# Optimization experiments

Measured on AMD Instinct MI355X. Metric: run time of the kernel, lower is better.

Reference implementation:

```python
import jax, jax.numpy as jnp
import numpy as np


def quantize_ternary(w):
    # BitNet b1.58 absmean ternary quantization: clip(round(w/gamma), -1, 1) * gamma
    gamma = jnp.mean(jnp.abs(w)) + 1e-8
    return jnp.clip(jnp.round(w / gamma), -1.0, 1.0) * gamma


def setup_inputs() -> dict:
    key = jax.random.key(0)
    k1, k2, k3, k4, k5 = jax.random.split(key, 5)
    B, T, E, D, H = 8, 2048, 8, 128, 512
    x = jax.random.normal(k1, (B, T, E, D), dtype=jnp.float32)
    expert_weights = jax.random.uniform(k2, (B, T, E), dtype=jnp.float32)
    # nn.init.uniform_(-1, 1)
    gate_weights = jax.random.uniform(k3, (E, H, D), dtype=jnp.float32, minval=-1.0, maxval=1.0)
    up_weights = jax.random.uniform(k4, (E, H, D), dtype=jnp.float32, minval=-1.0, maxval=1.0)
    down_weights = jax.random.uniform(k5, (E, D, H), dtype=jnp.float32, minval=-1.0, maxval=1.0)
    return {"x": x, "expert_weights": expert_weights, "gate_weights": gate_weights,
            "up_weights": up_weights, "down_weights": down_weights}


def reference(x, expert_weights, gate_weights, up_weights, down_weights):
    # Ternary-quantize all expert weights (dynamic absmean scale per tensor)
    gate_w = quantize_ternary(gate_weights)  # [E, H, D]
    up_w = quantize_ternary(up_weights)      # [E, H, D]
    down_w = quantize_ternary(down_weights)  # [E, D, H]

    gate_out = jnp.einsum('bted,ehd->bteh', x, gate_w)
    up_out = jnp.einsum('bted,ehd->bteh', x, up_w)
    hidden = jax.nn.silu(gate_out) * up_out          # SwiGLU gating
    output = jnp.einsum('bteh,edh->bted', hidden, down_w)
    return output * expert_weights[..., None]        # routing-weighted outputs
```

## Files before the change

kernel.cpp:

```cpp
#include <hip/hip_runtime.h>

typedef __attribute__((ext_vector_type(8)))  __bf16 bf16x8;
typedef __attribute__((ext_vector_type(16))) float  f32x16;

struct U4 { unsigned int x, y, z, w; };

static __device__ __forceinline__ unsigned short f2bf(float f){
  unsigned int u = __builtin_bit_cast(unsigned int, f);
  u += 0x7fffu + ((u >> 16) & 1u);
  return (unsigned short)(u >> 16);
}

static __device__ __forceinline__ unsigned pk2(float lo, float hi){
  return (unsigned)f2bf(lo) | ((unsigned)f2bf(hi) << 16);
}

static __device__ __forceinline__ bf16x8 ldfrag(const void* p){
  U4 v = *(const U4*)p;
  return __builtin_bit_cast(bf16x8, v);
}

static __device__ __forceinline__ f32x16 mfma32(bf16x8 a, bf16x8 b, f32x16 c){
  return __builtin_amdgcn_mfma_f32_32x32x16_bf16(a, b, c, 0, 0, 0);
}

static __device__ __forceinline__ f32x16 zero16(){
  f32x16 z;
#pragma unroll
  for (int i = 0; i < 16; ++i) z[i] = 0.0f;
  return z;
}

static __device__ __forceinline__ void gload16(const void* g, void* l){
  __builtin_amdgcn_global_load_lds(
      (const __attribute__((address_space(1))) unsigned int*)g,
      (__attribute__((address_space(3))) unsigned int*)l, 16, 0, 0);
}

static __device__ __forceinline__ void swap32(unsigned &a, unsigned &b){
  unsigned sa = (unsigned)__shfl_xor((int)a, 32, 64);
  unsigned sb = (unsigned)__shfl_xor((int)b, 32, 64);
  int l = (int)(threadIdx.x & 63);
  unsigned na = (l < 32) ? a : sb;
  unsigned nb = (l < 32) ? sa : b;
  a = na; b = nb;
}

#define IMG_EC  49152

__global__ void k_gamma(const float* __restrict__ gw, const float* __restrict__ uw,
                        const float* __restrict__ dw, float* __restrict__ sums){
  int t = blockIdx.y;
  const float* w = (t == 0) ? gw : (t == 1 ? uw : dw);
  int base = blockIdx.x * 2048 + threadIdx.x * 8;
  float4 a = *(const float4*)(w + base);
  float4 b = *(const float4*)(w + base + 4);
  float s = fabsf(a.x)+fabsf(a.y)+fabsf(a.z)+fabsf(a.w)
          + fabsf(b.x)+fabsf(b.y)+fabsf(b.z)+fabsf(b.w);
#pragma unroll
  for (int o = 32; o; o >>= 1) s += __shfl_xor(s, o);
  if ((threadIdx.x & 63) == 0) atomicAdd(&sums[t], s);
}

__global__ void k_quant(const float* __restrict__ gw, const float* __restrict__ uw,
                        const float* __restrict__ dw, const float* __restrict__ sums,
                        unsigned char* __restrict__ img){
  int b  = blockIdx.x;
  int tt = b % 3;
  int c  = (b / 3) & 7;
  int e  = b / 24;
  const float* w = (tt == 0) ? gw : (tt == 1 ? uw : dw);
  float inv = 1.0f / (sums[tt] * (1.0f / 524288.0f) + 1e-8f);
  unsigned char* dst = img + (size_t)(e * 8 + c) * IMG_EC + tt * 16384;
#pragma unroll
  for (int i = 0; i < 4; ++i){
    int grp = threadIdx.x + i * 256;
    int L = grp & 63, blkid = grp >> 6;
    int srcoff;
    if (tt < 2){
      int ht = blkid >> 3, ks = blkid & 7;
      int h  = c * 64 + ht * 32 + (L & 31);
      int dd = ks * 16 + (L >> 5) * 8;
      srcoff = (e * 512 + h) * 128 + dd;
    } else {
      int dt = blkid >> 2, ksp = blkid & 3;
      int d0 = dt * 32 + (L & 31);
      int h  = c * 64 + ksp * 16 + (L >> 5) * 8;
      srcoff = (e * 128 + d0) * 512 + h;
    }
    float4 f0 = *(const float4*)(w + srcoff);
    float4 f1 = *(const float4*)(w + srcoff + 4);
    float v[8] = {f0.x,f0.y,f0.z,f0.w,f1.x,f1.y,f1.z,f1.w};
    unsigned int o[4];
#pragma unroll
    for (int j = 0; j < 4; ++j){
      float q0 = fminf(1.0f, fmaxf(-1.0f, rintf(v[2*j]   * inv)));
      float q1 = fminf(1.0f, fmaxf(-1.0f, rintf(v[2*j+1] * inv)));
      o[j] = (unsigned int)f2bf(q0) | ((unsigned int)f2bf(q1) << 16);
    }
    *(U4*)(dst + grp * 16) = U4{o[0], o[1], o[2], o[3]};
  }
}

__global__ __attribute__((amdgpu_waves_per_eu(2, 2))) __launch_bounds__(512)
void k_moe(const float* __restrict__ x, const float* __restrict__ ew,
           const float* __restrict__ sums, const unsigned char* __restrict__ img,
           float* __restrict__ out){
  extern __shared__ char smem[];
  const int tile = blockIdx.x;
  const int e    = blockIdx.y;
  const int tid  = threadIdx.x;
  const int lane = tid & 63;
  const int wid  = tid >> 6;
  const int col  = lane & 31;
  const int hi   = lane >> 5;
  const int token = tile * 256 + wid * 32 + col;

  const float gg  = sums[0] * (1.0f/524288.0f) + 1e-8f;
  const float gu  = sums[1] * (1.0f/524288.0f) + 1e-8f;
  const float gdn = sums[2] * (1.0f/524288.0f) + 1e-8f;

  const unsigned char* wsrc0 = img + (size_t)e * 8 * IMG_EC;

#pragma unroll
  for (int i = 0; i < 6; ++i)
    gload16(wsrc0 + (size_t)(tid + i * 512) * 16, smem + (tid + i * 512) * 16);

  const float* xrow = x + ((size_t)token * 8 + e) * 128 + hi * 8;
  bf16x8 xf[8];
#pragma unroll
  for (int ks = 0; ks < 8; ++ks){
    float4 f0 = *(const float4*)(xrow + ks * 16);
    float4 f1 = *(const float4*)(xrow + ks * 16 + 4);
    U4 u{pk2(f0.x,f0.y), pk2(f0.z,f0.w), pk2(f1.x,f1.y), pk2(f1.z,f1.w)};
    xf[ks] = __builtin_bit_cast(bf16x8, u);
  }

  f32x16 O0 = zero16(), O1 = zero16(), O2 = zero16(), O3 = zero16();

  __syncthreads();

#pragma unroll 2
  for (int c = 0; c < 8; ++c){
    const char* cur = smem + (c & 1) * 49152;
    if (c < 7){
      const unsigned char* wsrc = wsrc0 + (size_t)(c + 1) * IMG_EC;
      char* nxt = smem + ((c + 1) & 1) * 49152;
#pragma unroll
      for (int i = 0; i < 6; ++i)
        gload16(wsrc + (size_t)(tid + i * 512) * 16, nxt + (tid + i * 512) * 16);
    }

    bf16x8 hf[4];
#pragma unroll
    for (int ht = 0; ht < 2; ++ht){
      f32x16 Cg = zero16(), Cu = zero16();
#pragma unroll
      for (int ks = 0; ks < 8; ++ks){
        bf16x8 ag = ldfrag(cur +         ((ht * 8 + ks) * 64 + lane) * 16);
        bf16x8 au = ldfrag(cur + 16384 + ((ht * 8 + ks) * 64 + lane) * 16);
        Cg = mfma32(ag, xf[ks], Cg);
        Cu = mfma32(au, xf[ks], Cu);
      }
#pragma unroll
      for (int s = 0; s < 2; ++s){
        float h[8];
#pragma unroll
        for (int j = 0; j < 8; ++j){
          float gv = Cg[s * 8 + j] * gg;
          float uv = Cu[s * 8 + j] * gu;
          h[j] = gv * __builtin_amdgcn_rcpf(1.0f + __expf(-gv)) * uv;
        }
        unsigned w0 = pk2(h[0], h[1]);
        unsigned w1 = pk2(h[2], h[3]);
        unsigned w2 = pk2(h[4], h[5]);
        unsigned w3 = pk2(h[6], h[7]);
        swap32(w0, w2);
        swap32(w1, w3);
        U4 u{w0, w1, w2, w3};
        hf[ht * 2 + s] = __builtin_bit_cast(bf16x8, u);
      }
    }

#pragma unroll
    for (int ks2 = 0; ks2 < 4; ++ks2){
      bf16x8 d0 = ldfrag(cur + 32768 + ((0 * 4 + ks2) * 64 + lane) * 16);
      bf16x8 d1 = ldfrag(cur + 32768 + ((1 * 4 + ks2) * 64 + lane) * 16);
      bf16x8 d2 = ldfrag(cur + 32768 + ((2 * 4 + ks2) * 64 + lane) * 16);
      bf16x8 d3 = ldfrag(cur + 32768 + ((3 * 4 + ks2) * 64 + lane) * 16);
      O0 = mfma32(d0, hf[ks2], O0);
      O1 = mfma32(d1, hf[ks2], O1);
      O2 = mfma32(d2, hf[ks2], O2);
      O3 = mfma32(d3, hf[ks2], O3);
    }

    if (c < 7) __syncthreads();
  }

  const float osc = gdn * ew[token * 8 + e];
  float* orow = out + ((size_t)token * 8 + e) * 128 + hi * 4;
#pragma unroll
  for (int dt = 0; dt < 4; ++dt){
    const f32x16& O = dt == 0 ? O0 : dt == 1 ? O1 : dt == 2 ? O2 : O3;
#pragma unroll
    for (int q = 0; q < 4; ++q){
      float4 v{O[q*4+0]*osc, O[q*4+1]*osc, O[q*4+2]*osc, O[q*4+3]*osc};
      *(float4*)(orow + dt * 32 + q * 8) = v;
    }
  }
}

extern "C" void kernel_launch(void* const* d_in, const int* in_sizes, int n_in,
                              void* d_out, int out_size, void* d_ws, size_t ws_size,
                              hipStream_t stream){
  const float* x  = (const float*)d_in[0];
  const float* ew = (const float*)d_in[1];
  const float* gw = (const float*)d_in[2];
  const float* uw = (const float*)d_in[3];
  const float* dw = (const float*)d_in[4];
  float* out = (float*)d_out;

  float* sums = (float*)d_ws;
  unsigned char* img = (unsigned char*)d_ws + 256;

  hipMemsetAsync(d_ws, 0, 16, stream);
  k_gamma<<<dim3(256, 3), 256, 0, stream>>>(gw, uw, dw, sums);
  k_quant<<<dim3(192), 256, 0, stream>>>(gw, uw, dw, sums, img);
  k_moe<<<dim3(64, 8), 512, 98304, stream>>>(x, ew, sums, img, out);
}
```

Before: 177.1 us.

## Software-pipeline down-projection one chunk behind and stage weights through registers

Replaces the direct global-to-LDS async loads with register-staged prefetch, where weights are loaded two chunks ahead into registers and then written to LDS. The down-projection for chunk i-1 is interleaved with the gate/up MFMAs of chunk i, with hidden fragments double-buffered and down weights triple-buffered in LDS. The aim is to overlap the SiLU/pack ALU work with the MFMA work and hide load latency. In exchange it raises register pressure and LDS use (112KB), which could limit occupancy or cause spills.

```diff
diff --git a/kernel.cpp b/kernel.cpp
--- a/kernel.cpp
+++ b/kernel.cpp
@@ -29,12 +29,6 @@
 #pragma unroll
   for (int i = 0; i < 16; ++i) z[i] = 0.0f;
   return z;
-}
-
-static __device__ __forceinline__ void gload16(const void* g, void* l){
-  __builtin_amdgcn_global_load_lds(
-      (const __attribute__((address_space(1))) unsigned int*)g,
-      (__attribute__((address_space(3))) unsigned int*)l, 16, 0, 0);
 }
 
 static __device__ __forceinline__ void swap32(unsigned &a, unsigned &b){
@@ -107,6 +101,8 @@
            const float* __restrict__ sums, const unsigned char* __restrict__ img,
            float* __restrict__ out){
   extern __shared__ char smem[];
+  char* GU = smem;
+  char* DN = smem + 65536;
   const int tile = blockIdx.x;
   const int e    = blockIdx.y;
   const int tid  = threadIdx.x;
@@ -122,10 +118,6 @@
 
   const unsigned char* wsrc0 = img + (size_t)e * 8 * IMG_EC;
 
-#pragma unroll
-  for (int i = 0; i < 6; ++i)
-    gload16(wsrc0 + (size_t)(tid + i * 512) * 16, smem + (tid + i * 512) * 16);
-
   const float* xrow = x + ((size_t)token * 8 + e) * 128 + hi * 8;
   bf16x8 xf[8];
 #pragma unroll
@@ -136,65 +128,103 @@
     xf[ks] = __builtin_bit_cast(bf16x8, u);
   }
 
+  U4 sg[4], sd[2];
+#pragma unroll
+  for (int k = 0; k < 4; ++k) sg[k] = *(const U4*)(wsrc0 + tid*16 + k*8192);
+#pragma unroll
+  for (int k = 0; k < 2; ++k) sd[k] = *(const U4*)(wsrc0 + 32768 + tid*16 + k*8192);
+#pragma unroll
+  for (int k = 0; k < 4; ++k) *(U4*)(GU + tid*16 + k*8192) = sg[k];
+#pragma unroll
+  for (int k = 0; k < 2; ++k) *(U4*)(DN + tid*16 + k*8192) = sd[k];
+#pragma unroll
+  for (int k = 0; k < 4; ++k) sg[k] = *(const U4*)(wsrc0 + IMG_EC + tid*16 + k*8192);
+#pragma unroll
+  for (int k = 0; k < 2; ++k) sd[k] = *(const U4*)(wsrc0 + IMG_EC + 32768 + tid*16 + k*8192);
+  __syncthreads();
+
   f32x16 O0 = zero16(), O1 = zero16(), O2 = zero16(), O3 = zero16();
-
-  __syncthreads();
-
-#pragma unroll 2
-  for (int c = 0; c < 8; ++c){
-    const char* cur = smem + (c & 1) * 49152;
-    if (c < 7){
-      const unsigned char* wsrc = wsrc0 + (size_t)(c + 1) * IMG_EC;
-      char* nxt = smem + ((c + 1) & 1) * 49152;
-#pragma unroll
-      for (int i = 0; i < 6; ++i)
-        gload16(wsrc + (size_t)(tid + i * 512) * 16, nxt + (tid + i * 512) * 16);
-    }
-
-    bf16x8 hf[4];
-#pragma unroll
-    for (int ht = 0; ht < 2; ++ht){
-      f32x16 Cg = zero16(), Cu = zero16();
-#pragma unroll
-      for (int ks = 0; ks < 8; ++ks){
-        bf16x8 ag = ldfrag(cur +         ((ht * 8 + ks) * 64 + lane) * 16);
-        bf16x8 au = ldfrag(cur + 16384 + ((ht * 8 + ks) * 64 + lane) * 16);
-        Cg = mfma32(ag, xf[ks], Cg);
-        Cu = mfma32(au, xf[ks], Cu);
+  bf16x8 hf[2][4];
+
+#pragma unroll
+  for (int i = 0; i < 9; ++i){
+    if (i < 7){
+      char* gub = GU + ((i+1)&1) * 32768;
+      char* dnb = DN + ((i+1)%3) * 16384;
+#pragma unroll
+      for (int k = 0; k < 4; ++k) *(U4*)(gub + tid*16 + k*8192) = sg[k];
+#pragma unroll
+      for (int k = 0; k < 2; ++k) *(U4*)(dnb + tid*16 + k*8192) = sd[k];
+    }
+    if (i < 6){
+      const unsigned char* cs = wsrc0 + (size_t)(i+2) * IMG_EC;
+#pragma unroll
+      for (int k = 0; k < 4; ++k) sg[k] = *(const U4*)(cs + tid*16 + k*8192);
+#pragma unroll
+      for (int k = 0; k < 2; ++k) sd[k] = *(const U4*)(cs + 32768 + tid*16 + k*8192);
+    }
+
+    if (i < 8){
+      const char* gub = GU + (i&1) * 32768;
+      const char* dnb = DN + ((i-1+3)%3) * 16384;
+#pragma unroll
+      for (int ht = 0; ht < 2; ++ht){
+        f32x16 Cg = zero16(), Cu = zero16();
+#pragma unroll
+        for (int ks = 0; ks < 8; ++ks){
+          bf16x8 ag = ldfrag(gub +         ((ht*8 + ks)*64 + lane)*16);
+          bf16x8 au = ldfrag(gub + 16384 + ((ht*8 + ks)*64 + lane)*16);
+          Cg = mfma32(ag, xf[ks], Cg);
+          Cu = mfma32(au, xf[ks], Cu);
+        }
+        if (i >= 1){
+#pragma unroll
+          for (int ks2 = 0; ks2 < 4; ++ks2){
+            bf16x8 dA = ldfrag(dnb + (((ht*2+0)*4 + ks2)*64 + lane)*16);
+            bf16x8 dB = ldfrag(dnb + (((ht*2+1)*4 + ks2)*64 + lane)*16);
+            if (ht == 0){
+              O0 = mfma32(dA, hf[(i-1)&1][ks2], O0);
+              O1 = mfma32(dB, hf[(i-1)&1][ks2], O1);
+            } else {
+              O2 = mfma32(dA, hf[(i-1)&1][ks2], O2);
+              O3 = mfma32(dB, hf[(i-1)&1][ks2], O3);
+            }
+          }
+        }
+#pragma unroll
+        for (int s = 0; s < 2; ++s){
+          float h[8];
+#pragma unroll
+          for (int j = 0; j < 8; ++j){
+            float gv = Cg[s*8 + j] * gg;
+            float uv = Cu[s*8 + j] * gu;
+            h[j] = gv * __builtin_amdgcn_rcpf(1.0f + __expf(-gv)) * uv;
+          }
+          unsigned w0 = pk2(h[0], h[1]);
+          unsigned w1 = pk2(h[2], h[3]);
+          unsigned w2 = pk2(h[4], h[5]);
+          unsigned w3 = pk2(h[6], h[7]);
+          swap32(w0, w2);
+          swap32(w1, w3);
+          U4 u{w0, w1, w2, w3};
+          hf[i&1][ht*2 + s] = __builtin_bit_cast(bf16x8, u);
+        }
       }
-#pragma unroll
-      for (int s = 0; s < 2; ++s){
-        float h[8];
-#pragma unroll
-        for (int j = 0; j < 8; ++j){
-          float gv = Cg[s * 8 + j] * gg;
-          float uv = Cu[s * 8 + j] * gu;
-          h[j] = gv * __builtin_amdgcn_rcpf(1.0f + __expf(-gv)) * uv;
-        }
-        unsigned w0 = pk2(h[0], h[1]);
-        unsigned w1 = pk2(h[2], h[3]);
-        unsigned w2 = pk2(h[4], h[5]);
-        unsigned w3 = pk2(h[6], h[7]);
-        swap32(w0, w2);
-        swap32(w1, w3);
-        U4 u{w0, w1, w2, w3};
-        hf[ht * 2 + s] = __builtin_bit_cast(bf16x8, u);
+    } else {
+      const char* dnb = DN + (7%3) * 16384;
+#pragma unroll
+      for (int ks2 = 0; ks2 < 4; ++ks2){
+        bf16x8 d0 = ldfrag(dnb + ((0*4 + ks2)*64 + lane)*16);
+        bf16x8 d1 = ldfrag(dnb + ((1*4 + ks2)*64 + lane)*16);
+        bf16x8 d2 = ldfrag(dnb + ((2*4 + ks2)*64 + lane)*16);
+        bf16x8 d3 = ldfrag(dnb + ((3*4 + ks2)*64 + lane)*16);
+        O0 = mfma32(d0, hf[1][ks2], O0);
+        O1 = mfma32(d1, hf[1][ks2], O1);
+        O2 = mfma32(d2, hf[1][ks2], O2);
+        O3 = mfma32(d3, hf[1][ks2], O3);
       }
     }
-
-#pragma unroll
-    for (int ks2 = 0; ks2 < 4; ++ks2){
-      bf16x8 d0 = ldfrag(cur + 32768 + ((0 * 4 + ks2) * 64 + lane) * 16);
-      bf16x8 d1 = ldfrag(cur + 32768 + ((1 * 4 + ks2) * 64 + lane) * 16);
-      bf16x8 d2 = ldfrag(cur + 32768 + ((2 * 4 + ks2) * 64 + lane) * 16);
-      bf16x8 d3 = ldfrag(cur + 32768 + ((3 * 4 + ks2) * 64 + lane) * 16);
-      O0 = mfma32(d0, hf[ks2], O0);
-      O1 = mfma32(d1, hf[ks2], O1);
-      O2 = mfma32(d2, hf[ks2], O2);
-      O3 = mfma32(d3, hf[ks2], O3);
-    }
-
-    if (c < 7) __syncthreads();
+    if (i < 8) __syncthreads();
   }
 
   const float osc = gdn * ew[token * 8 + e];
@@ -226,5 +256,5 @@
   hipMemsetAsync(d_ws, 0, 16, stream);
   k_gamma<<<dim3(256, 3), 256, 0, stream>>>(gw, uw, dw, sums);
   k_quant<<<dim3(192), 256, 0, stream>>>(gw, uw, dw, sums, img);
-  k_moe<<<dim3(64, 8), 512, 98304, stream>>>(x, ew, sums, img, out);
-}
+  k_moe<<<dim3(64, 8), 512, 114688, stream>>>(x, ew, sums, img, out);
+}
```

Result: slower. 239.7 us (+35.3%).

## Replace LDS double buffer with register-staged single buffer and native bf16 converts

Applied to the files above, without the earlier changes.

Swaps the direct global-to-LDS double-buffered weight prefetch (96KB dynamic LDS) for a single static 48KB LDS buffer. The next chunk is prefetched into registers and written to LDS after a barrier. It also drops the waves_per_eu(2,2) constraint, uses the hardware bf16 conversion instead of manual rounding, and uses v_permlane32_swap in place of the two shuffles plus selects. Halving LDS may allow more resident blocks per CU, but it adds a second barrier per iteration and raises register pressure from the 6 staged U4 values.

```diff
diff --git a/kernel.cpp b/kernel.cpp
--- a/kernel.cpp
+++ b/kernel.cpp
@@ -5,14 +5,10 @@
 
 struct U4 { unsigned int x, y, z, w; };
 
-static __device__ __forceinline__ unsigned short f2bf(float f){
-  unsigned int u = __builtin_bit_cast(unsigned int, f);
-  u += 0x7fffu + ((u >> 16) & 1u);
-  return (unsigned short)(u >> 16);
-}
-
 static __device__ __forceinline__ unsigned pk2(float lo, float hi){
-  return (unsigned)f2bf(lo) | ((unsigned)f2bf(hi) << 16);
+  unsigned short ul = __builtin_bit_cast(unsigned short, (__bf16)lo);
+  unsigned short uh = __builtin_bit_cast(unsigned short, (__bf16)hi);
+  return (unsigned)ul | ((unsigned)uh << 16);
 }
 
 static __device__ __forceinline__ bf16x8 ldfrag(const void* p){
@@ -31,19 +27,8 @@
   return z;
 }
 
-static __device__ __forceinline__ void gload16(const void* g, void* l){
-  __builtin_amdgcn_global_load_lds(
-      (const __attribute__((address_space(1))) unsigned int*)g,
-      (__attribute__((address_space(3))) unsigned int*)l, 16, 0, 0);
-}
-
 static __device__ __forceinline__ void swap32(unsigned &a, unsigned &b){
-  unsigned sa = (unsigned)__shfl_xor((int)a, 32, 64);
-  unsigned sb = (unsigned)__shfl_xor((int)b, 32, 64);
-  int l = (int)(threadIdx.x & 63);
-  unsigned na = (l < 32) ? a : sb;
-  unsigned nb = (l < 32) ? sa : b;
-  a = na; b = nb;
+  asm volatile("v_permlane32_swap_b32 %0, %1" : "+v"(a), "+v"(b));
 }
 
 #define IMG_EC  49152
@@ -96,17 +81,17 @@
     for (int j = 0; j < 4; ++j){
       float q0 = fminf(1.0f, fmaxf(-1.0f, rintf(v[2*j]   * inv)));
       float q1 = fminf(1.0f, fmaxf(-1.0f, rintf(v[2*j+1] * inv)));
-      o[j] = (unsigned int)f2bf(q0) | ((unsigned int)f2bf(q1) << 16);
+      o[j] = pk2(q0, q1);
     }
     *(U4*)(dst + grp * 16) = U4{o[0], o[1], o[2], o[3]};
   }
 }
 
-__global__ __attribute__((amdgpu_waves_per_eu(2, 2))) __launch_bounds__(512)
+__global__ __launch_bounds__(512)
 void k_moe(const float* __restrict__ x, const float* __restrict__ ew,
            const float* __restrict__ sums, const unsigned char* __restrict__ img,
            float* __restrict__ out){
-  extern __shared__ char smem[];
+  __shared__ char WB[49152];
   const int tile = blockIdx.x;
   const int e    = blockIdx.y;
   const int tid  = threadIdx.x;
@@ -122,9 +107,10 @@
 
   const unsigned char* wsrc0 = img + (size_t)e * 8 * IMG_EC;
 
-#pragma unroll
-  for (int i = 0; i < 6; ++i)
-    gload16(wsrc0 + (size_t)(tid + i * 512) * 16, smem + (tid + i * 512) * 16);
+  U4 stg[6];
+#pragma unroll
+  for (int k = 0; k < 6; ++k)
+    stg[k] = *(const U4*)(wsrc0 + tid * 16 + k * 8192);
 
   const float* xrow = x + ((size_t)token * 8 + e) * 128 + hi * 8;
   bf16x8 xf[8];
@@ -138,17 +124,18 @@
 
   f32x16 O0 = zero16(), O1 = zero16(), O2 = zero16(), O3 = zero16();
 
-  __syncthreads();
-
-#pragma unroll 2
   for (int c = 0; c < 8; ++c){
-    const char* cur = smem + (c & 1) * 49152;
+    if (c) __syncthreads();
+#pragma unroll
+    for (int k = 0; k < 6; ++k)
+      *(U4*)(WB + tid * 16 + k * 8192) = stg[k];
+    __syncthreads();
+
     if (c < 7){
-      const unsigned char* wsrc = wsrc0 + (size_t)(c + 1) * IMG_EC;
-      char* nxt = smem + ((c + 1) & 1) * 49152;
-#pragma unroll
-      for (int i = 0; i < 6; ++i)
-        gload16(wsrc + (size_t)(tid + i * 512) * 16, nxt + (tid + i * 512) * 16);
+      const unsigned char* cs = wsrc0 + (size_t)(c + 1) * IMG_EC;
+#pragma unroll
+      for (int k = 0; k < 6; ++k)
+        stg[k] = *(const U4*)(cs + tid * 16 + k * 8192);
     }
 
     bf16x8 hf[4];
@@ -157,8 +144,8 @@
       f32x16 Cg = zero16(), Cu = zero16();
 #pragma unroll
       for (int ks = 0; ks < 8; ++ks){
-        bf16x8 ag = ldfrag(cur +         ((ht * 8 + ks) * 64 + lane) * 16);
-        bf16x8 au = ldfrag(cur + 16384 + ((ht * 8 + ks) * 64 + lane) * 16);
+        bf16x8 ag = ldfrag(WB +         ((ht*8 + ks)*64 + lane)*16);
+        bf16x8 au = ldfrag(WB + 16384 + ((ht*8 + ks)*64 + lane)*16);
         Cg = mfma32(ag, xf[ks], Cg);
         Cu = mfma32(au, xf[ks], Cu);
       }
@@ -167,8 +154,8 @@
         float h[8];
 #pragma unroll
         for (int j = 0; j < 8; ++j){
-          float gv = Cg[s * 8 + j] * gg;
-          float uv = Cu[s * 8 + j] * gu;
+          float gv = Cg[s*8 + j] * gg;
+          float uv = Cu[s*8 + j] * gu;
           h[j] = gv * __builtin_amdgcn_rcpf(1.0f + __expf(-gv)) * uv;
         }
         unsigned w0 = pk2(h[0], h[1]);
@@ -178,23 +165,21 @@
         swap32(w0, w2);
         swap32(w1, w3);
         U4 u{w0, w1, w2, w3};
-        hf[ht * 2 + s] = __builtin_bit_cast(bf16x8, u);
+        hf[ht*2 + s] = __builtin_bit_cast(bf16x8, u);
       }
     }
 
 #pragma unroll
     for (int ks2 = 0; ks2 < 4; ++ks2){
-      bf16x8 d0 = ldfrag(cur + 32768 + ((0 * 4 + ks2) * 64 + lane) * 16);
-      bf16x8 d1 = ldfrag(cur + 32768 + ((1 * 4 + ks2) * 64 + lane) * 16);
-      bf16x8 d2 = ldfrag(cur + 32768 + ((2 * 4 + ks2) * 64 + lane) * 16);
-      bf16x8 d3 = ldfrag(cur + 32768 + ((3 * 4 + ks2) * 64 + lane) * 16);
+      bf16x8 d0 = ldfrag(WB + 32768 + ((0*4 + ks2)*64 + lane)*16);
+      bf16x8 d1 = ldfrag(WB + 32768 + ((1*4 + ks2)*64 + lane)*16);
+      bf16x8 d2 = ldfrag(WB + 32768 + ((2*4 + ks2)*64 + lane)*16);
+      bf16x8 d3 = ldfrag(WB + 32768 + ((3*4 + ks2)*64 + lane)*16);
       O0 = mfma32(d0, hf[ks2], O0);
       O1 = mfma32(d1, hf[ks2], O1);
       O2 = mfma32(d2, hf[ks2], O2);
       O3 = mfma32(d3, hf[ks2], O3);
     }
-
-    if (c < 7) __syncthreads();
   }
 
   const float osc = gdn * ew[token * 8 + e];
@@ -226,5 +211,5 @@
   hipMemsetAsync(d_ws, 0, 16, stream);
   k_gamma<<<dim3(256, 3), 256, 0, stream>>>(gw, uw, dw, sums);
   k_quant<<<dim3(192), 256, 0, stream>>>(gw, uw, dw, sums, img);
-  k_moe<<<dim3(64, 8), 512, 98304, stream>>>(x, ew, sums, img, out);
-}
+  k_moe<<<dim3(64, 8), 512, 0, stream>>>(x, ew, sums, img, out);
+}
```

Result: no change. 178.5 us (+0.8%).
